# Kernel optimization log

Hardware: AMD Instinct MI355X
Metric: run time of the kernel (lower is better)

Reference implementation:

```python
import jax, jax.numpy as jnp
import numpy as np

D_MODEL = 1024
N_HEAD = 16
ATT_DIM = D_MODEL // N_HEAD  # 64
B, S = 8, 2048


def setup_inputs() -> dict:
    key = jax.random.key(0)
    kq, kk, kv, kwq, kwk, kwv = jax.random.split(key, 6)
    # xavier_uniform bound for Linear(hidden_dim -> att_dim)
    bound = float(np.sqrt(6.0 / (D_MODEL + ATT_DIM)))
    return {
        "q": jax.random.normal(kq, (B, S, D_MODEL), dtype=jnp.float32),
        "k": jax.random.normal(kk, (B, S, D_MODEL), dtype=jnp.float32),
        "v": jax.random.normal(kv, (B, S, D_MODEL), dtype=jnp.float32),
        "Wq": jax.random.uniform(kwq, (ATT_DIM, D_MODEL), jnp.float32, -bound, bound),
        "Wk": jax.random.uniform(kwk, (ATT_DIM, D_MODEL), jnp.float32, -bound, bound),
        "Wv": jax.random.uniform(kwv, (ATT_DIM, D_MODEL), jnp.float32, -bound, bound),
    }


def reference(q, k, v, Wq, Wk, Wv):
    # Linear projections (no bias): [B,S,d_model] @ [d_model,att_dim]
    qp = jnp.einsum('bsd,ed->bse', q, Wq)
    kp = jnp.einsum('bsd,ed->bse', k, Wk)
    vp = jnp.einsum('bsd,ed->bse', v, Wv)
    # Scores: note original divides by att_dim (not sqrt)
    scores = jnp.einsum('bqe,bke->bqk', qp, kp) / ATT_DIM
    probs = jax.nn.softmax(scores, axis=-1)  # [B,S,S]
    att = jnp.einsum('bqk,bke->bqe', probs, vp)  # [B,S,att_dim]
    # dropout is identity in eval mode
    return (att, probs)
```

## Files before the change

### kernel.cpp

```cpp
#include <hip/hip_runtime.h>
#include <hip/hip_bf16.h>

#define D_MODEL 1024
#define ATT_DIM 64
#define BATCH 8
#define SEQ 2048
#define MROWS (BATCH * SEQ)

typedef short bf16x8 __attribute__((ext_vector_type(8)));
typedef float f32x4 __attribute__((ext_vector_type(4)));

#define MFMA16(a, b, c) __builtin_amdgcn_mfma_f32_16x16x32_bf16((a), (b), (c), 0, 0, 0)

__device__ inline short f2bf(float f) {
    union { __hip_bfloat16 h; short s; } u;
    u.h = __float2bfloat16(f);
    return u.s;
}

__device__ __forceinline__ unsigned cvtpk(float lo, float hi) {
    unsigned r;
    asm("v_cvt_pk_bf16_f32 %0, %1, %2" : "=v"(r) : "v"(lo), "v"(hi));
    return r;
}

__device__ __forceinline__ void gload_lds16(const void* g, void* l) {
    __builtin_amdgcn_global_load_lds(
        (const __attribute__((address_space(1))) void*)g,
        (__attribute__((address_space(3))) void*)l, 16, 0, 0);
}

__global__ __launch_bounds__(256) void wcvt_kernel(
    const float* __restrict__ Wq, const float* __restrict__ Wk,
    const float* __restrict__ Wv, short* __restrict__ Wbf)
{
    const int idx = blockIdx.x * 256 + threadIdx.x;
    const int per = ATT_DIM * D_MODEL;
    const int base = idx * 8;
    const int mi = base / per;
    const int off = base - mi * per;
    const float* src = (mi == 0) ? Wq : (mi == 1 ? Wk : Wv);
    const float sc = (mi == 0) ? (1.0f / 64.0f) : 1.0f;
    const float4 a = *reinterpret_cast<const float4*>(src + off);
    const float4 b = *reinterpret_cast<const float4*>(src + off + 4);
    bf16x8 r;
    r[0] = f2bf(a.x * sc); r[1] = f2bf(a.y * sc);
    r[2] = f2bf(a.z * sc); r[3] = f2bf(a.w * sc);
    r[4] = f2bf(b.x * sc); r[5] = f2bf(b.y * sc);
    r[6] = f2bf(b.z * sc); r[7] = f2bf(b.w * sc);
    *reinterpret_cast<bf16x8*>(Wbf + base) = r;
}

__global__ __launch_bounds__(256) void proj_mfma_kernel(
    const float* __restrict__ q, const float* __restrict__ k,
    const float* __restrict__ v, const short* __restrict__ Wbf,
    short* __restrict__ qp, short* __restrict__ kp, short* __restrict__ vpT)
{
    const int mat = blockIdx.y;
    const float* x = (mat == 0) ? q : (mat == 1 ? k : v);
    const short* W = Wbf + mat * ATT_DIM * D_MODEL;

    __shared__ float As[3][4096];
    __shared__ short Ws[3][4096];

    const int tid = threadIdx.x;
    const int w = tid >> 6;
    const int l = tid & 63;
    const int lr = l & 15;
    const int g = l >> 4;

    const int m0 = blockIdx.x * 64;
    const int row = w * 16 + lr;
    const int xrA = (row & 7) << 4;
    const int xrW = (lr & 7) << 4;

    f32x4 acc[4] = {};

    #define STAGE_A(c, buf)                                                    \
        {                                                                      \
            _Pragma("unroll")                                                  \
            for (int j = 0; j < 4; ++j) {                                      \
                const int rs = (w * 4 + j) * 4 + g;                            \
                const int scb = (lr * 16) ^ ((rs & 7) << 4);                   \
                gload_lds16(x + (long)(m0 + rs) * D_MODEL + (c) * 64 + (scb >> 2), \
                            &As[buf][(w * 4 + j) * 256]);                      \
            }                                                                  \
        }
    #define STAGE_W(c, buf)                                                    \
        {                                                                      \
            _Pragma("unroll")                                                  \
            for (int j = 0; j < 2; ++j) {                                      \
                const int rW = (w * 2 + j) * 8 + (l >> 3);                     \
                const int sb = ((l & 7) * 16) ^ ((rW & 7) << 4);               \
                gload_lds16(W + rW * D_MODEL + (c) * 64 + (sb >> 1),           \
                            &Ws[buf][(w * 2 + j) * 512]);                      \
            }                                                                  \
        }

    STAGE_A(0, 0); STAGE_W(0, 0);
    STAGE_A(1, 1); STAGE_W(1, 1);

    #pragma unroll
    for (int c = 0; c < 16; ++c) {
        const int buf = c % 3;
        if (c < 15) asm volatile("s_waitcnt vmcnt(6)" ::: "memory");
        else        asm volatile("s_waitcnt vmcnt(0)" ::: "memory");
        __builtin_amdgcn_sched_barrier(0);
        __builtin_amdgcn_s_barrier();
        __builtin_amdgcn_sched_barrier(0);

        const char* Ab = (const char*)&As[buf][0] + row * 256;
        const char* Wb = (const char*)&Ws[buf][0];
        #pragma unroll
        for (int ks = 0; ks < 2; ++ks) {
            const int b0 = ks * 128 + g * 32;
            const float4 a0 = *reinterpret_cast<const float4*>(Ab + (b0 ^ xrA));
            const float4 a1 = *reinterpret_cast<const float4*>(Ab + ((b0 + 16) ^ xrA));
            bf16x8 af;
            af[0] = f2bf(a0.x); af[1] = f2bf(a0.y); af[2] = f2bf(a0.z); af[3] = f2bf(a0.w);
            af[4] = f2bf(a1.x); af[5] = f2bf(a1.y); af[6] = f2bf(a1.z); af[7] = f2bf(a1.w);
            const int cbw = (ks * 64 + g * 16);
            #pragma unroll
            for (int ef = 0; ef < 4; ++ef) {
                const bf16x8 wf = *reinterpret_cast<const bf16x8*>(
                    Wb + (ef * 16 + lr) * 128 + (cbw ^ xrW));
                acc[ef] = MFMA16(af, wf, acc[ef]);
            }
        }
        if (c <= 13) { STAGE_A(c + 2, (c + 2) % 3); STAGE_W(c + 2, (c + 2) % 3); }
    }
    #undef STAGE_A
    #undef STAGE_W

    if (mat < 2) {
        short* out = (mat == 0) ? qp : kp;
        #pragma unroll
        for (int ef = 0; ef < 4; ++ef)
            #pragma unroll
            for (int j = 0; j < 4; ++j)
                out[(long)(m0 + w * 16 + g * 4 + j) * ATT_DIM + ef * 16 + lr] =
                    f2bf(acc[ef][j]);
    } else {
        const int b = m0 / SEQ;
        const int s0 = (m0 - b * SEQ) + w * 16;
        #pragma unroll
        for (int ef = 0; ef < 4; ++ef)
            #pragma unroll
            for (int j = 0; j < 4; ++j)
                vpT[((long)b * ATT_DIM + ef * 16 + lr) * SEQ + s0 + g * 4 + j] =
                    f2bf(acc[ef][j]);
    }
}

__global__ __launch_bounds__(512, 4) void attn_kernel(
    const short* __restrict__ qp, const short* __restrict__ kp,
    const short* __restrict__ vpT, float* __restrict__ probs,
    float* __restrict__ att)
{
    __shared__ float stats_l[8][16];
    __shared__ float lds_o[8][64][17];

    const int tid = threadIdx.x;
    const int w = tid >> 6;
    const int l = tid & 63;
    const int lr = l & 15;
    const int g = l >> 4;

    const int b = blockIdx.y;
    const int q0 = blockIdx.x * 16;

    const short* qpb = qp + ((long)b * SEQ + q0) * ATT_DIM;
    const short* kpb = kp + (long)b * SEQ * ATT_DIM;
    const short* vTb = vpT + (long)b * ATT_DIM * SEQ;

    const bf16x8 qa0 = *reinterpret_cast<const bf16x8*>(qpb + lr * ATT_DIM + g * 8);
    const bf16x8 qa1 = *reinterpret_cast<const bf16x8*>(qpb + lr * ATT_DIM + 32 + g * 8);

    const int kbeg = w * 256;

    f32x4 s[8][2];
    #pragma unroll
    for (int ch = 0; ch < 8; ++ch) {
        const short* kb = kpb + (long)(kbeg + ch * 32) * ATT_DIM;
        const bf16x8 kb00 = *reinterpret_cast<const bf16x8*>(kb + lr * ATT_DIM + g * 8);
        const bf16x8 kb01 = *reinterpret_cast<const bf16x8*>(kb + lr * ATT_DIM + 32 + g * 8);
        const bf16x8 kb10 = *reinterpret_cast<const bf16x8*>(kb + (16 + lr) * ATT_DIM + g * 8);
        const bf16x8 kb11 = *reinterpret_cast<const bf16x8*>(kb + (16 + lr) * ATT_DIM + 32 + g * 8);
        f32x4 t0 = {}; t0 = MFMA16(kb00, qa0, t0); t0 = MFMA16(kb01, qa1, t0);
        f32x4 t1 = {}; t1 = MFMA16(kb10, qa0, t1); t1 = MFMA16(kb11, qa1, t1);
        s[ch][0] = t0; s[ch][1] = t1;
    }

    float lw = 0.f;
    #pragma unroll
    for (int ch = 0; ch < 8; ++ch)
        #pragma unroll
        for (int h = 0; h < 2; ++h)
            #pragma unroll
            for (int j = 0; j < 4; ++j) {
                const float e = __expf(s[ch][h][j]);
                s[ch][h][j] = e;
                lw += e;
            }
    lw += __shfl_xor(lw, 16);
    lw += __shfl_xor(lw, 32);

    if (l < 16) stats_l[w][l] = lw;
    __syncthreads();

    float tot = 0.f;
    #pragma unroll
    for (int ww = 0; ww < 8; ++ww) tot += stats_l[ww][lr];
    const float inv = 1.0f / tot;
    #pragma unroll
    for (int ch = 0; ch < 8; ++ch)
        #pragma unroll
        for (int h = 0; h < 2; ++h)
            s[ch][h] *= inv;

    f32x4 accO[4] = {};
    float* pbase = probs + ((long)b * SEQ + q0 + lr) * SEQ;
    const bool hi2 = (g & 2) != 0;
    const bool swp = ((g ^ (g >> 1)) & 1) != 0;
    const bool odd = (g & 1) != 0;

    #pragma unroll
    for (int ch = 0; ch < 8; ++ch) {
        const int k0 = kbeg + ch * 32;
        *reinterpret_cast<f32x4*>(pbase + k0 + g * 4)      = s[ch][0];
        *reinterpret_cast<f32x4*>(pbase + k0 + 16 + g * 4) = s[ch][1];

        const unsigned xy0 = cvtpk(s[ch][0][0], s[ch][0][1]);
        const unsigned xy1 = cvtpk(s[ch][0][2], s[ch][0][3]);
        const unsigned zw0 = cvtpk(s[ch][1][0], s[ch][1][1]);
        const unsigned zw1 = cvtpk(s[ch][1][2], s[ch][1][3]);

        const unsigned s1a = hi2 ? xy0 : zw0;
        const unsigned s1b = hi2 ? xy1 : zw1;
        const unsigned r1a = __shfl_xor(s1a, 32);
        const unsigned r1b = __shfl_xor(s1b, 32);
        const unsigned p1a = hi2 ? zw0 : xy0;
        const unsigned p1b = hi2 ? zw1 : xy1;
        const unsigned s2a = swp ? p1a : r1a;
        const unsigned s2b = swp ? p1b : r1b;
        const unsigned r2a = __shfl_xor(s2a, 16);
        const unsigned r2b = __shfl_xor(s2b, 16);
        const unsigned ka = swp ? r1a : p1a;
        const unsigned kb_ = swp ? r1b : p1b;
        const unsigned d0 = odd ? r2a : ka;
        const unsigned d1 = odd ? r2b : kb_;
        const unsigned d2 = odd ? ka : r2a;
        const unsigned d3 = odd ? kb_ : r2b;
        union { uint4 u4; bf16x8 v; } pbu;
        pbu.u4 = make_uint4(d0, d1, d2, d3);
        const bf16x8 pb = pbu.v;

        #pragma unroll
        for (int ef = 0; ef < 4; ++ef) {
            const bf16x8 va = *reinterpret_cast<const bf16x8*>(
                vTb + (long)(ef * 16 + lr) * SEQ + k0 + g * 8);
            accO[ef] = MFMA16(va, pb, accO[ef]);
        }
    }

    #pragma unroll
    for (int ef = 0; ef < 4; ++ef)
        #pragma unroll
        for (int j = 0; j < 4; ++j)
            lds_o[w][ef * 16 + g * 4 + j][lr] = accO[ef][j];
    __syncthreads();

    {
        const int qr = tid >> 5;
        const int e0 = (tid & 31) * 2;
        float o0 = 0.f, o1 = 0.f;
        #pragma unroll
        for (int ww = 0; ww < 8; ++ww) {
            o0 += lds_o[ww][e0][qr];
            o1 += lds_o[ww][e0 + 1][qr];
        }
        float2 o = make_float2(o0, o1);
        *reinterpret_cast<float2*>(att + ((long)b * SEQ + q0 + qr) * ATT_DIM + e0) = o;
    }
}

extern "C" void kernel_launch(void* const* d_in, const int* in_sizes, int n_in,
                              void* d_out, int out_size, void* d_ws, size_t ws_size,
                              hipStream_t stream)
{
    const float* q  = (const float*)d_in[0];
    const float* k  = (const float*)d_in[1];
    const float* v  = (const float*)d_in[2];
    const float* Wq = (const float*)d_in[3];
    const float* Wk = (const float*)d_in[4];
    const float* Wv = (const float*)d_in[5];

    float* att   = (float*)d_out;
    float* probs = att + (size_t)BATCH * SEQ * ATT_DIM;

    short* qp  = (short*)d_ws;
    short* kp  = qp + (size_t)MROWS * ATT_DIM;
    short* vpT = kp + (size_t)MROWS * ATT_DIM;
    short* Wbf = vpT + (size_t)MROWS * ATT_DIM;

    wcvt_kernel<<<dim3(96), 256, 0, stream>>>(Wq, Wk, Wv, Wbf);

    proj_mfma_kernel<<<dim3(MROWS / 64, 3), 256, 0, stream>>>(
        q, k, v, Wbf, qp, kp, vpT);

    attn_kernel<<<dim3(SEQ / 16, BATCH), 512, 0, stream>>>(
        qp, kp, vpT, probs, att);
}
```

Measured before the change: 141.8 us.

## Load projection operands directly into registers instead of LDS staging

The projection kernel drops its LDS triple-buffered global_load_lds staging and barriers. Each wave now loads its own 16 rows of activations and the bf16 weight fragments straight into registers, double-buffered two chunks ahead, and converts with packed bf16 conversions. Blocks shrink to 128 threads covering 32 rows, so the grid doubles. This removes LDS traffic and workgroup barriers, at the cost of each wave re-reading the weights from L1/L2 and using more registers.

```diff
diff --git a/kernel.cpp b/kernel.cpp
--- a/kernel.cpp
+++ b/kernel.cpp
@@ -22,12 +22,6 @@
     unsigned r;
     asm("v_cvt_pk_bf16_f32 %0, %1, %2" : "=v"(r) : "v"(lo), "v"(hi));
     return r;
-}
-
-__device__ __forceinline__ void gload_lds16(const void* g, void* l) {
-    __builtin_amdgcn_global_load_lds(
-        (const __attribute__((address_space(1))) void*)g,
-        (__attribute__((address_space(3))) void*)l, 16, 0, 0);
 }
 
 __global__ __launch_bounds__(256) void wcvt_kernel(
@@ -51,7 +45,7 @@
     *reinterpret_cast<bf16x8*>(Wbf + base) = r;
 }
 
-__global__ __launch_bounds__(256) void proj_mfma_kernel(
+__global__ __launch_bounds__(128) void proj_mfma_kernel(
     const float* __restrict__ q, const float* __restrict__ k,
     const float* __restrict__ v, const short* __restrict__ Wbf,
     short* __restrict__ qp, short* __restrict__ kp, short* __restrict__ vpT)
@@ -59,9 +53,6 @@
     const int mat = blockIdx.y;
     const float* x = (mat == 0) ? q : (mat == 1 ? k : v);
     const short* W = Wbf + mat * ATT_DIM * D_MODEL;
-
-    __shared__ float As[3][4096];
-    __shared__ short Ws[3][4096];
 
     const int tid = threadIdx.x;
     const int w = tid >> 6;
@@ -69,68 +60,52 @@
     const int lr = l & 15;
     const int g = l >> 4;
 
-    const int m0 = blockIdx.x * 64;
-    const int row = w * 16 + lr;
-    const int xrA = (row & 7) << 4;
-    const int xrW = (lr & 7) << 4;
+    const int m0 = blockIdx.x * 32 + w * 16;
+    const float* xrow = x + (long)(m0 + lr) * D_MODEL + g * 8;
+    const short* wbase = W + lr * D_MODEL + g * 8;
 
     f32x4 acc[4] = {};
-
-    #define STAGE_A(c, buf)                                                    \
+    float4 ar[2][4];
+    bf16x8 wr[2][8];
+
+    #define LOAD(bank, c)                                                      \
         {                                                                      \
             _Pragma("unroll")                                                  \
-            for (int j = 0; j < 4; ++j) {                                      \
-                const int rs = (w * 4 + j) * 4 + g;                            \
-                const int scb = (lr * 16) ^ ((rs & 7) << 4);                   \
-                gload_lds16(x + (long)(m0 + rs) * D_MODEL + (c) * 64 + (scb >> 2), \
-                            &As[buf][(w * 4 + j) * 256]);                      \
+            for (int ks = 0; ks < 2; ++ks) {                                   \
+                _Pragma("unroll")                                              \
+                for (int h = 0; h < 2; ++h)                                    \
+                    ar[bank][ks * 2 + h] = *reinterpret_cast<const float4*>(   \
+                        xrow + (c) * 64 + ks * 32 + h * 4);                    \
+                _Pragma("unroll")                                              \
+                for (int ef = 0; ef < 4; ++ef)                                 \
+                    wr[bank][ks * 4 + ef] = *reinterpret_cast<const bf16x8*>(  \
+                        wbase + ef * 16 * D_MODEL + (c) * 64 + ks * 32);       \
             }                                                                  \
         }
-    #define STAGE_W(c, buf)                                                    \
-        {                                                                      \
-            _Pragma("unroll")                                                  \
-            for (int j = 0; j < 2; ++j) {                                      \
-                const int rW = (w * 2 + j) * 8 + (l >> 3);                     \
-                const int sb = ((l & 7) * 16) ^ ((rW & 7) << 4);               \
-                gload_lds16(W + rW * D_MODEL + (c) * 64 + (sb >> 1),           \
-                            &Ws[buf][(w * 2 + j) * 512]);                      \
-            }                                                                  \
-        }
-
-    STAGE_A(0, 0); STAGE_W(0, 0);
-    STAGE_A(1, 1); STAGE_W(1, 1);
+
+    LOAD(0, 0);
+    LOAD(1, 1);
 
     #pragma unroll
     for (int c = 0; c < 16; ++c) {
-        const int buf = c % 3;
-        if (c < 15) asm volatile("s_waitcnt vmcnt(6)" ::: "memory");
-        else        asm volatile("s_waitcnt vmcnt(0)" ::: "memory");
-        __builtin_amdgcn_sched_barrier(0);
-        __builtin_amdgcn_s_barrier();
-        __builtin_amdgcn_sched_barrier(0);
-
-        const char* Ab = (const char*)&As[buf][0] + row * 256;
-        const char* Wb = (const char*)&Ws[buf][0];
+        const int bk = c & 1;
         #pragma unroll
         for (int ks = 0; ks < 2; ++ks) {
-            const int b0 = ks * 128 + g * 32;
-            const float4 a0 = *reinterpret_cast<const float4*>(Ab + (b0 ^ xrA));
-            const float4 a1 = *reinterpret_cast<const float4*>(Ab + ((b0 + 16) ^ xrA));
-            bf16x8 af;
-            af[0] = f2bf(a0.x); af[1] = f2bf(a0.y); af[2] = f2bf(a0.z); af[3] = f2bf(a0.w);
-            af[4] = f2bf(a1.x); af[5] = f2bf(a1.y); af[6] = f2bf(a1.z); af[7] = f2bf(a1.w);
-            const int cbw = (ks * 64 + g * 16);
-            #pragma unroll
-            for (int ef = 0; ef < 4; ++ef) {
-                const bf16x8 wf = *reinterpret_cast<const bf16x8*>(
-                    Wb + (ef * 16 + lr) * 128 + (cbw ^ xrW));
-                acc[ef] = MFMA16(af, wf, acc[ef]);
-            }
-        }
-        if (c <= 13) { STAGE_A(c + 2, (c + 2) % 3); STAGE_W(c + 2, (c + 2) % 3); }
-    }
-    #undef STAGE_A
-    #undef STAGE_W
+            const float4 a0 = ar[bk][ks * 2];
+            const float4 a1 = ar[bk][ks * 2 + 1];
+            union { uint4 u4; bf16x8 v8; } afu;
+            afu.u4.x = cvtpk(a0.x, a0.y);
+            afu.u4.y = cvtpk(a0.z, a0.w);
+            afu.u4.z = cvtpk(a1.x, a1.y);
+            afu.u4.w = cvtpk(a1.z, a1.w);
+            const bf16x8 af = afu.v8;
+            #pragma unroll
+            for (int ef = 0; ef < 4; ++ef)
+                acc[ef] = MFMA16(af, wr[bk][ks * 4 + ef], acc[ef]);
+        }
+        if (c <= 13) LOAD(bk, c + 2);
+    }
+    #undef LOAD
 
     if (mat < 2) {
         short* out = (mat == 0) ? qp : kp;
@@ -138,11 +113,11 @@
         for (int ef = 0; ef < 4; ++ef)
             #pragma unroll
             for (int j = 0; j < 4; ++j)
-                out[(long)(m0 + w * 16 + g * 4 + j) * ATT_DIM + ef * 16 + lr] =
+                out[(long)(m0 + g * 4 + j) * ATT_DIM + ef * 16 + lr] =
                     f2bf(acc[ef][j]);
     } else {
         const int b = m0 / SEQ;
-        const int s0 = (m0 - b * SEQ) + w * 16;
+        const int s0 = m0 - b * SEQ;
         #pragma unroll
         for (int ef = 0; ef < 4; ++ef)
             #pragma unroll
@@ -305,7 +280,7 @@
 
     wcvt_kernel<<<dim3(96), 256, 0, stream>>>(Wq, Wk, Wv, Wbf);
 
-    proj_mfma_kernel<<<dim3(MROWS / 64, 3), 256, 0, stream>>>(
+    proj_mfma_kernel<<<dim3(MROWS / 32, 3), 128, 0, stream>>>(
         q, k, v, Wbf, qp, kp, vpT);
 
     attn_kernel<<<dim3(SEQ / 16, BATCH), 512, 0, stream>>>(
```

Result: slower. 166.9 us (+17.7%).

## Simplify projection kernel to 128-thread blocks with double-buffered activations only

Applied to the files above, without the earlier changes.

The projection kernel is restructured. Blocks now cover 32 rows with 128 threads instead of 64 rows with 256 threads. The triple-buffered LDS pipeline, with explicit vmcnt waits, is replaced by a double buffer using __syncthreads. The bf16 weights are no longer staged in LDS and are read directly from global memory (L2) inside the MFMA loop. This cuts LDS use and doubles the number of blocks to improve occupancy, but each block now fetches the weights from global memory and the pipeline has less latency hiding.

```diff
diff --git a/kernel.cpp b/kernel.cpp
--- a/kernel.cpp
+++ b/kernel.cpp
@@ -51,7 +51,7 @@
     *reinterpret_cast<bf16x8*>(Wbf + base) = r;
 }
 
-__global__ __launch_bounds__(256) void proj_mfma_kernel(
+__global__ __launch_bounds__(128) void proj_mfma_kernel(
     const float* __restrict__ q, const float* __restrict__ k,
     const float* __restrict__ v, const short* __restrict__ Wbf,
     short* __restrict__ qp, short* __restrict__ kp, short* __restrict__ vpT)
@@ -60,8 +60,7 @@
     const float* x = (mat == 0) ? q : (mat == 1 ? k : v);
     const short* W = Wbf + mat * ATT_DIM * D_MODEL;
 
-    __shared__ float As[3][4096];
-    __shared__ short Ws[3][4096];
+    __shared__ float As[2][2048];
 
     const int tid = threadIdx.x;
     const int w = tid >> 6;
@@ -69,68 +68,51 @@
     const int lr = l & 15;
     const int g = l >> 4;
 
-    const int m0 = blockIdx.x * 64;
+    const int m0 = blockIdx.x * 32;
     const int row = w * 16 + lr;
-    const int xrA = (row & 7) << 4;
-    const int xrW = (lr & 7) << 4;
+    const int xr = (row & 7) << 4;
 
     f32x4 acc[4] = {};
 
-    #define STAGE_A(c, buf)                                                    \
+    #define STAGE(c, buf)                                                      \
         {                                                                      \
+            const int kt_ = (c) * 64;                                          \
             _Pragma("unroll")                                                  \
             for (int j = 0; j < 4; ++j) {                                      \
                 const int rs = (w * 4 + j) * 4 + g;                            \
                 const int scb = (lr * 16) ^ ((rs & 7) << 4);                   \
-                gload_lds16(x + (long)(m0 + rs) * D_MODEL + (c) * 64 + (scb >> 2), \
+                gload_lds16(x + (long)(m0 + rs) * D_MODEL + kt_ + (scb >> 2),  \
                             &As[buf][(w * 4 + j) * 256]);                      \
             }                                                                  \
         }
-    #define STAGE_W(c, buf)                                                    \
-        {                                                                      \
-            _Pragma("unroll")                                                  \
-            for (int j = 0; j < 2; ++j) {                                      \
-                const int rW = (w * 2 + j) * 8 + (l >> 3);                     \
-                const int sb = ((l & 7) * 16) ^ ((rW & 7) << 4);               \
-                gload_lds16(W + rW * D_MODEL + (c) * 64 + (sb >> 1),           \
-                            &Ws[buf][(w * 2 + j) * 512]);                      \
-            }                                                                  \
-        }
-
-    STAGE_A(0, 0); STAGE_W(0, 0);
-    STAGE_A(1, 1); STAGE_W(1, 1);
-
-    #pragma unroll
+
+    STAGE(0, 0);
+    __syncthreads();
+
     for (int c = 0; c < 16; ++c) {
-        const int buf = c % 3;
-        if (c < 15) asm volatile("s_waitcnt vmcnt(6)" ::: "memory");
-        else        asm volatile("s_waitcnt vmcnt(0)" ::: "memory");
-        __builtin_amdgcn_sched_barrier(0);
-        __builtin_amdgcn_s_barrier();
-        __builtin_amdgcn_sched_barrier(0);
-
+        const int buf = c & 1;
+        if (c < 15) STAGE(c + 1, buf ^ 1);
+
+        const int kt = c * 64;
         const char* Ab = (const char*)&As[buf][0] + row * 256;
-        const char* Wb = (const char*)&Ws[buf][0];
         #pragma unroll
         for (int ks = 0; ks < 2; ++ks) {
             const int b0 = ks * 128 + g * 32;
-            const float4 a0 = *reinterpret_cast<const float4*>(Ab + (b0 ^ xrA));
-            const float4 a1 = *reinterpret_cast<const float4*>(Ab + ((b0 + 16) ^ xrA));
+            const float4 a0 = *reinterpret_cast<const float4*>(Ab + (b0 ^ xr));
+            const float4 a1 = *reinterpret_cast<const float4*>(Ab + ((b0 + 16) ^ xr));
             bf16x8 af;
             af[0] = f2bf(a0.x); af[1] = f2bf(a0.y); af[2] = f2bf(a0.z); af[3] = f2bf(a0.w);
             af[4] = f2bf(a1.x); af[5] = f2bf(a1.y); af[6] = f2bf(a1.z); af[7] = f2bf(a1.w);
-            const int cbw = (ks * 64 + g * 16);
             #pragma unroll
             for (int ef = 0; ef < 4; ++ef) {
                 const bf16x8 wf = *reinterpret_cast<const bf16x8*>(
-                    Wb + (ef * 16 + lr) * 128 + (cbw ^ xrW));
+                    W + (ef * 16 + lr) * D_MODEL + kt + ks * 32 + g * 8);
                 acc[ef] = MFMA16(af, wf, acc[ef]);
             }
         }
-        if (c <= 13) { STAGE_A(c + 2, (c + 2) % 3); STAGE_W(c + 2, (c + 2) % 3); }
-    }
-    #undef STAGE_A
-    #undef STAGE_W
+        __syncthreads();
+    }
+    #undef STAGE
 
     if (mat < 2) {
         short* out = (mat == 0) ? qp : kp;
@@ -305,7 +287,7 @@
 
     wcvt_kernel<<<dim3(96), 256, 0, stream>>>(Wq, Wk, Wv, Wbf);
 
-    proj_mfma_kernel<<<dim3(MROWS / 64, 3), 256, 0, stream>>>(
+    proj_mfma_kernel<<<dim3(MROWS / 32, 3), 128, 0, stream>>>(
         q, k, v, Wbf, qp, kp, vpT);
 
     attn_kernel<<<dim3(SEQ / 16, BATCH), 512, 0, stream>>>(
```

Result: slower. 147.7 us (+4.1%).
